# Optimization experiments

Hardware: AMD Instinct MI355X
Metric: run time of the kernel (lower is better)

The kernel has to match this reference:

```python
import jax, jax.numpy as jnp
import numpy as np

N_CELLS, D_IN, D_HID, D_OUT, MLP_W = 16384, 512, 1024, 512, 128
N_FACTIONS, SYNC, DEBATE = 8, 0.15, 0.15


def setup_inputs() -> dict:
    key = jax.random.key(0)
    ks = jax.random.split(key, 20)
    s = 0.05
    inp = {
        "x": jax.random.normal(ks[0], (1, D_IN), jnp.float32),
        "hiddens": jax.random.normal(ks[1], (N_CELLS, D_HID), jnp.float32) * 0.1,
        "wealth_norm": jax.random.uniform(ks[2], (N_CELLS,), jnp.float32, 0.5, 1.5),
        "Wa1": jax.random.normal(ks[3], (D_IN + D_HID, MLP_W), jnp.float32) * s,
        "ba1": jax.random.normal(ks[4], (MLP_W,), jnp.float32) * s,
        "Wa2": jax.random.normal(ks[5], (MLP_W, D_OUT), jnp.float32) * s,
        "ba2": jax.random.normal(ks[6], (D_OUT,), jnp.float32) * s,
        "Wg1": jax.random.normal(ks[7], (D_IN + D_HID, MLP_W), jnp.float32) * s,
        "bg1": jax.random.normal(ks[8], (MLP_W,), jnp.float32) * s,
        "Wg2": jax.random.normal(ks[9], (MLP_W, D_OUT), jnp.float32) * s,
        "bg2": jax.random.normal(ks[10], (D_OUT,), jnp.float32) * s,
        "W_ih": jax.random.normal(ks[11], (D_OUT + 1, 3 * D_HID), jnp.float32) * s,
        "W_hh": jax.random.normal(ks[12], (D_HID, 3 * D_HID), jnp.float32) * s,
        "b_ih": jax.random.normal(ks[13], (3 * D_HID,), jnp.float32) * s,
        "b_hh": jax.random.normal(ks[14], (3 * D_HID,), jnp.float32) * s,
        "Wo": jax.random.normal(ks[15], (D_OUT, D_IN), jnp.float32) * s,
        "bo": jax.random.normal(ks[16], (D_IN,), jnp.float32) * s,
        "positions": jax.random.randint(ks[17], (N_CELLS,), 0, 3, jnp.int32) - 1,
        "step": 10,
    }
    return inp


def _gru_cell(mem, h, W_ih, W_hh, b_ih, b_hh):
    # torch.nn.GRUCell math, gate order r, z, n
    gi = mem @ W_ih + b_ih            # [N, 3H]
    gh = h @ W_hh + b_hh              # [N, 3H]
    gi_r, gi_z, gi_n = jnp.split(gi, 3, axis=-1)
    gh_r, gh_z, gh_n = jnp.split(gh, 3, axis=-1)
    r = jax.nn.sigmoid(gi_r + gh_r)
    z = jax.nn.sigmoid(gi_z + gh_z)
    n = jnp.tanh(gi_n + r * gh_n)
    return (1.0 - z) * n + z * h


def _group_sync(h, mask):
    cnt = jnp.sum(mask)
    m = mask[:, None].astype(h.dtype)
    mean = jnp.sum(h * m, axis=0) / jnp.maximum(cnt, 1).astype(h.dtype)
    blended = 0.9 * h + 0.1 * mean
    return jnp.where((mask[:, None]) & (cnt >= 2), blended, h)


def _faction_sync_debate(h, step):
    n = h.shape[0]
    n_f = min(N_FACTIONS, n // 2)
    if n_f < 2:
        return h
    fs = n // n_f
    hf = h[: n_f * fs].reshape(n_f, fs, -1)
    fmean = hf.mean(axis=1, keepdims=True)                    # [n_f, 1, H]
    hf = (1.0 - SYNC) * hf + SYNC * fmean
    if step > 5:
        global_op = hf.mean(axis=1).mean(axis=0)              # [H]
        dc = max(1, fs // 4)
        head = (1.0 - DEBATE) * hf[:, :dc] + DEBATE * global_op
        hf = jnp.concatenate([head, hf[:, dc:]], axis=1)
    out = hf.reshape(n_f * fs, -1)
    if n_f * fs < n:
        out = jnp.concatenate([out, h[n_f * fs:]], axis=0)
    return out


def reference(x, hiddens, wealth_norm, Wa1, ba1, Wa2, ba2, Wg1, bg1, Wg2, bg2,
              W_ih, W_hh, b_ih, b_hh, Wo, bo, positions, step):
    n = hiddens.shape[0]
    xb = jnp.broadcast_to(x, (n, x.shape[-1]))                # same x for every cell
    combined = jnp.concatenate([xb, hiddens], axis=-1)        # [N, D_in+D_hid]
    a = jax.nn.relu(combined @ Wa1 + ba1) @ Wa2 + ba2
    g = jax.nn.relu(combined @ Wg1 + bg1) @ Wg2 + bg2
    output = a - g                                            # [N, D_out]
    tension = jnp.mean(output ** 2, axis=-1, keepdims=True)   # [N, 1]
    mem_input = jax.lax.stop_gradient(jnp.concatenate([output, tension], axis=-1))
    new_h = _gru_cell(mem_input, hiddens, W_ih, W_hh, b_ih, b_hh)
    mod = 0.9 + 0.1 * jnp.clip(wealth_norm, 0.1, 2.0)
    new_h = jnp.clip(new_h * mod[:, None], -10.0, 10.0)
    new_h = jax.lax.stop_gradient(new_h)                      # original detaches state
    new_h = _group_sync(new_h, positions > 0)
    new_h = _group_sync(new_h, positions < 0)
    new_h = _faction_sync_debate(new_h, step)
    # tension weights come from .item() in torch -> constants
    weights = jax.nn.softmax(jax.lax.stop_gradient(tension[:, 0]))
    combined_out = weights @ output                           # [D_out]
    pred = (combined_out @ Wo + bo)[None, :]                  # [1, D_in]
    avg_tension = jnp.mean(tension)
    return pred, avg_tension, new_h
```

## Files before the change

### kernel.cpp

```cpp
#include <hip/hip_runtime.h>
#include <stdint.h>

typedef unsigned short u16;
typedef __bf16 bf16x8 __attribute__((ext_vector_type(8)));
typedef float f32x4 __attribute__((ext_vector_type(4)));


__device__ __forceinline__ float bf2f(unsigned u) { return __uint_as_float(u << 16); }
__device__ __forceinline__ u16 f2bf(float f) {
  unsigned x = __float_as_uint(f);
  unsigned r = x + 0x7fffu + ((x >> 16) & 1u);
  return (u16)(r >> 16);
}
__device__ __forceinline__ unsigned pack2(float a, float b) {
  return (unsigned)f2bf(a) | ((unsigned)f2bf(b) << 16);
}
__device__ __forceinline__ float sigm(float x) { return 1.f / (1.f + __expf(-x)); }
__device__ __forceinline__ float fast_tanh(float x) {
  float e = __expf(2.f * x);
  return 1.f - 2.f / (e + 1.f);
}

#define AS1(p) ((const __attribute__((address_space(1))) void*)(p))
#define AS3(p) ((__attribute__((address_space(3))) void*)(p))

#define NC 16384

__global__ __launch_bounds__(256) void prep_cvt(const float* __restrict__ hid,
                                                u16* __restrict__ hidc) {
  int b = blockIdx.x, t = threadIdx.x;
  const float4* src = (const float4*)hid;
  uint2* dst = (uint2*)hidc;
#pragma unroll
  for (int c = 0; c < 8; ++c) {
    float4 v = src[(size_t)(b + c * 2048) * 256 + t];
    uint2 o; o.x = pack2(v.x, v.y); o.y = pack2(v.z, v.w);
    dst[(size_t)(b + c * 2048) * 256 + t] = o;
  }
}

__device__ __forceinline__ void packT_body(
    const float* __restrict__ src, int sld, int srow0,
    u16* __restrict__ dst, int dld, int drow0, int koff,
    int remapThresh, int remapAdd, float sgn, int bx, int by,
    float (*tile)[65], int t) {
  const int k0 = by * 64, c0 = bx * 64;
  const int tx = t & 15, ty = t >> 4;
#pragma unroll
  for (int p = 0; p < 4; ++p) {
    int r = ty + p * 16;
    float4 v = *reinterpret_cast<const float4*>(&src[(size_t)(srow0 + k0 + r) * sld + c0 + tx * 4]);
    tile[tx * 4 + 0][r] = v.x;
    tile[tx * 4 + 1][r] = v.y;
    tile[tx * 4 + 2][r] = v.z;
    tile[tx * 4 + 3][r] = v.w;
  }
  __syncthreads();
  const int cl = t >> 2;
  const int kb = (t & 3) * 16;
  int col = c0 + cl;
  int row = drow0 + col + ((col >= remapThresh) ? remapAdd : 0);
  union { u16 o[16]; uint4 v[2]; } u;
#pragma unroll
  for (int e = 0; e < 16; ++e) u.o[e] = f2bf(sgn * tile[cl][kb + e]);
  uint4* d = reinterpret_cast<uint4*>(&dst[(size_t)row * dld + koff + k0 + kb]);
  d[0] = u.v[0]; d[1] = u.v[1];
}

__global__ __launch_bounds__(256) void prep_packT(
    const float* __restrict__ W_ih, const float* __restrict__ W_hh, u16* __restrict__ WgruT,
    const float* __restrict__ Wa1, const float* __restrict__ Wg1, u16* __restrict__ W1catT,
    const float* __restrict__ Wa2, const float* __restrict__ Wg2, u16* __restrict__ W2catT) {
  __shared__ float tile[64][65];
  int b = blockIdx.x, t = threadIdx.x;
  if (b < 768) {
    packT_body(W_hh, 3072, 0, WgruT, 1536, 0, 512, 2048, 1024, 1.f, b % 48, b / 48, tile, t);
    return;
  }
  b -= 768;
  if (b < 384) {
    packT_body(W_ih, 3072, 0, WgruT, 1536, 0, 0, 1 << 30, 0, 1.f, b % 48, b / 48, tile, t);
    return;
  }
  b -= 384;
  if (b < 32) { packT_body(Wa1, 128, 512, W1catT, 1024, 0, 0, 1 << 30, 0, 1.f, b % 2, b / 2, tile, t); return; }
  b -= 32;
  if (b < 32) { packT_body(Wg1, 128, 512, W1catT, 1024, 128, 0, 1 << 30, 0, 1.f, b % 2, b / 2, tile, t); return; }
  b -= 32;
  if (b < 16) { packT_body(Wa2, 512, 0, W2catT, 256, 0, 0, 1 << 30, 0, 1.f, b % 8, b / 8, tile, t); return; }
  b -= 16;
  { packT_body(Wg2, 512, 0, W2catT, 256, 0, 128, 1 << 30, 0, -1.f, b % 8, b / 8, tile, t); }
}

__global__ __launch_bounds__(256) void prep_small(
    const float* __restrict__ Wa1, const float* __restrict__ Wg1,
    const float* __restrict__ x, const float* __restrict__ ba1, const float* __restrict__ bg1,
    float* __restrict__ bias1, const float* __restrict__ ba2, const float* __restrict__ bg2,
    float* __restrict__ bias2, const int* __restrict__ positions, int* __restrict__ counts) {
  int b = blockIdx.x, t = threadIdx.x;
  if (b < 64) {
    const float* W = (t < 128) ? Wa1 : Wg1;
    int cc = t & 127;
    int k0 = b * 8;
    float wv[8], xv[8];
#pragma unroll
    for (int j = 0; j < 8; ++j) {
      xv[j] = x[k0 + j];
      wv[j] = W[(size_t)(k0 + j) * 128 + cc];
    }
    float acc = 0.f;
#pragma unroll
    for (int j = 0; j < 8; ++j) acc += xv[j] * wv[j];
    if (b == 0) acc += (t < 128) ? ba1[cc] : bg1[cc];
    atomicAdd(&bias1[t], acc);
    return;
  }
  b -= 64;
  if (b < 2) { int n = b * 256 + t; bias2[n] = ba2[n] - bg2[n]; return; }
  b -= 2;
  {
    int i = b * 256 + t;
    int p = positions[i], f = i >> 11;
    if (p > 0) atomicAdd(&counts[f * 2], 1);
    else if (p < 0) atomicAdd(&counts[f * 2 + 1], 1);
  }
}

__global__ __launch_bounds__(256) void gemm_bt(
    const u16* __restrict__ A, int lda,
    const u16* __restrict__ Bt, int ldb,
    u16* __restrict__ C, int ldc,
    const float* __restrict__ bias, int epi, int K,
    float* __restrict__ tension) {
  __shared__ __align__(16) u16 As[3][128 * 32];
  __shared__ __align__(16) u16 Bs[3][128 * 32];
  const int tid = threadIdx.x;
  const int m0 = blockIdx.x * 128;
  const int n0 = blockIdx.y * 128;
  f32x4 acc[4][4] = {};
  const int lane = tid & 63;
  const int w = tid >> 6;
  const int mw = (w & 1) * 64, nw = (w >> 1) * 64;
  const int fr = lane & 15;
  const int q = lane >> 4;
  const int ar0 = tid >> 2;
  const int ag = ((tid & 3) ^ ((ar0 >> 1) & 3)) * 8;

  const u16* aB0 = A + (size_t)(m0 + ar0) * lda + ag;
  const u16* aB1 = A + (size_t)(m0 + ar0 + 64) * lda + ag;
  const u16* bB0 = Bt + (size_t)(n0 + ar0) * ldb + ag;
  const u16* bB1 = Bt + (size_t)(n0 + ar0 + 64) * ldb + ag;

  auto stage = [&](int kk, int buf) {
    __builtin_amdgcn_global_load_lds(AS1(aB0 + kk), AS3(&As[buf][tid * 8]), 16, 0, 0);
    __builtin_amdgcn_global_load_lds(AS1(aB1 + kk), AS3(&As[buf][(tid + 256) * 8]), 16, 0, 0);
    __builtin_amdgcn_global_load_lds(AS1(bB0 + kk), AS3(&Bs[buf][tid * 8]), 16, 0, 0);
    __builtin_amdgcn_global_load_lds(AS1(bB1 + kk), AS3(&Bs[buf][(tid + 256) * 8]), 16, 0, 0);
  };

  const int NT = K >> 5;
  stage(0, 0);
  stage(32, 1);
  int cur = 0, nxt = 1, nx2 = 2;
#pragma unroll 1
  for (int t = 0; t < NT; ++t) {
    if (t + 2 < NT) stage((t + 2) * 32, nx2);
    const int rem = NT - 1 - t;
    if (rem >= 2)      asm volatile("s_waitcnt vmcnt(8)" ::: "memory");
    else if (rem == 1) asm volatile("s_waitcnt vmcnt(4)" ::: "memory");
    else               asm volatile("s_waitcnt vmcnt(0)" ::: "memory");
    __builtin_amdgcn_s_barrier();
    asm volatile("" ::: "memory");
    bf16x8 af[4], bfv[4];
#pragma unroll
    for (int mt = 0; mt < 4; ++mt) {
      int r = mw + mt * 16 + fr;
      af[mt] = *reinterpret_cast<const bf16x8*>(&As[cur][r * 32 + ((q ^ ((r >> 1) & 3)) * 8)]);
    }
#pragma unroll
    for (int nt = 0; nt < 4; ++nt) {
      int r = nw + nt * 16 + fr;
      bfv[nt] = *reinterpret_cast<const bf16x8*>(&Bs[cur][r * 32 + ((q ^ ((r >> 1) & 3)) * 8)]);
    }
    __builtin_amdgcn_s_setprio(1);
#pragma unroll
    for (int mt = 0; mt < 4; ++mt)
#pragma unroll
      for (int nt = 0; nt < 4; ++nt)
        acc[mt][nt] = __builtin_amdgcn_mfma_f32_16x16x32_bf16(af[mt], bfv[nt], acc[mt][nt], 0, 0, 0);
    __builtin_amdgcn_s_setprio(0);
    asm volatile("s_waitcnt lgkmcnt(0)" ::: "memory");
    __builtin_amdgcn_s_barrier();
    int tmp = cur; cur = nxt; nxt = nx2; nx2 = tmp;
  }
  const int rq = q * 4;
#pragma unroll
  for (int mt = 0; mt < 4; ++mt) {
    float srow[4] = {0.f, 0.f, 0.f, 0.f};
#pragma unroll
    for (int nt = 0; nt < 4; ++nt) {
      int col = n0 + nw + nt * 16 + fr;
      f32x4 v = acc[mt][nt];
#pragma unroll
      for (int r = 0; r < 4; ++r) {
        int row = m0 + mw + mt * 16 + rq + r;
        float val = v[r] + bias[col];
        if (epi == 1) val = val > 0.f ? val : 0.f;
        else srow[r] += val * val;
        C[(size_t)row * ldc + col] = f2bf(val);
      }
    }
    if (epi == 3) {
#pragma unroll
      for (int r = 0; r < 4; ++r) {
        float s = srow[r];
        s += __shfl_xor(s, 1, 16); s += __shfl_xor(s, 2, 16);
        s += __shfl_xor(s, 4, 16); s += __shfl_xor(s, 8, 16);
        if (fr == 0) atomicAdd(&tension[m0 + mw + mt * 16 + rq + r], s);
      }
    }
  }
}

__global__ __launch_bounds__(256, 2) void gemm_gru(
    const u16* __restrict__ outbf, const u16* __restrict__ hidc,
    const u16* __restrict__ WgruT,
    const float* __restrict__ W_ihf, const float* __restrict__ bihf,
    const float* __restrict__ bhhf, const float* __restrict__ wealthf,
    const float* __restrict__ tension, u16* __restrict__ hpre) {
  __shared__ __align__(16) u16 As[2][128 * 64];
  __shared__ __align__(16) u16 Bs[2][3][64 * 64];
  const int tid = threadIdx.x;
  const int m0 = blockIdx.x * 128;
  const int j0 = blockIdx.y * 64;
  f32x4 acc[4][4][2] = {};
  const int lane = tid & 63;
  const int w = tid >> 6;
  const int mw = (w & 1) * 64, jw = (w >> 1) * 32;
  const int fr = lane & 15;
  const int q = lane >> 4;
  const int rowl = tid >> 3;
  const int koffT = ((tid & 7) ^ (rowl & 7)) * 8;
  const size_t aOutB = (size_t)(m0 + rowl) * 512 + koffT;
  const size_t aHidB = (size_t)(m0 + rowl) * 1024 + koffT;
  const size_t bB    = (size_t)(j0 + rowl) * 1536 + koffT;
  const int f7 = fr & 7;
  const int sk0 = (q ^ f7) * 8;
  const int sk1 = ((4 + q) ^ f7) * 8;

#define STAGE(S, BUF)                                                                              \
  {                                                                                                \
    const int s8 = (S) < 8 ? (S) : (S) - 8;                                                        \
    const size_t kO = (size_t)(S) * 64;                                                            \
    const size_t kOA = (size_t)s8 * 64;                                                            \
    if ((S) < 8) {                                                                                 \
      _Pragma("unroll") for (int it = 0; it < 4; ++it)                                             \
          __builtin_amdgcn_global_load_lds(AS1(outbf + aOutB + (size_t)(32 * it) * 512 + kOA),     \
                                           AS3(&As[BUF][tid * 8 + it * 2048]), 16, 0, 0);          \
    } else {                                                                                       \
      _Pragma("unroll") for (int it = 0; it < 4; ++it)                                             \
          __builtin_amdgcn_global_load_lds(AS1(hidc + aHidB + (size_t)(32 * it) * 1024 + kOA),     \
                                           AS3(&As[BUF][tid * 8 + it * 2048]), 16, 0, 0);          \
    }                                                                                              \
    const u16* bp = WgruT + bB + kO;                                                               \
    __builtin_amdgcn_global_load_lds(AS1(bp), AS3(&Bs[BUF][0][tid * 8]), 16, 0, 0);                \
    __builtin_amdgcn_global_load_lds(AS1(bp + (size_t)32 * 1536),                                  \
                                     AS3(&Bs[BUF][0][tid * 8 + 2048]), 16, 0, 0);                  \
    __builtin_amdgcn_global_load_lds(AS1(bp + (size_t)1024 * 1536),                                \
                                     AS3(&Bs[BUF][1][tid * 8]), 16, 0, 0);                         \
    __builtin_amdgcn_global_load_lds(AS1(bp + (size_t)1056 * 1536),                                \
                                     AS3(&Bs[BUF][1][tid * 8 + 2048]), 16, 0, 0);                  \
    const size_t nOff = ((S) < 8 ? (size_t)2048 * 1536 : (size_t)3072 * 1536);                     \
    __builtin_amdgcn_global_load_lds(AS1(bp + nOff), AS3(&Bs[BUF][2][tid * 8]), 16, 0, 0);         \
    __builtin_amdgcn_global_load_lds(AS1(bp + nOff + (size_t)32 * 1536),                           \
                                     AS3(&Bs[BUF][2][tid * 8 + 2048]), 16, 0, 0);                  \
  }

#define GRU_STEP(T, REG3, CUR)                                                                     \
  {                                                                                                \
    bf16x8 af0[4], b00[2], b10[2], b20[2];                                                         \
    _Pragma("unroll") for (int mt = 0; mt < 4; ++mt)                                               \
        af0[mt] = *reinterpret_cast<const bf16x8*>(&As[CUR][(mw + mt * 16 + fr) * 64 + sk0]);      \
    _Pragma("unroll") for (int nt = 0; nt < 2; ++nt) {                                             \
      int rj = (jw + nt * 16 + fr) * 64 + sk0;                                                     \
      b00[nt] = *reinterpret_cast<const bf16x8*>(&Bs[CUR][0][rj]);                                 \
      b10[nt] = *reinterpret_cast<const bf16x8*>(&Bs[CUR][1][rj]);                                 \
      b20[nt] = *reinterpret_cast<const bf16x8*>(&Bs[CUR][2][rj]);                                 \
    }                                                                                              \
    __builtin_amdgcn_s_setprio(1);                                                                 \
    _Pragma("unroll") for (int mt = 0; mt < 4; ++mt)                                               \
        _Pragma("unroll") for (int nt = 0; nt < 2; ++nt) {                                         \
      acc[0][mt][nt] = __builtin_amdgcn_mfma_f32_16x16x32_bf16(af0[mt], b00[nt], acc[0][mt][nt], 0, 0, 0); \
      acc[1][mt][nt] = __builtin_amdgcn_mfma_f32_16x16x32_bf16(af0[mt], b10[nt], acc[1][mt][nt], 0, 0, 0); \
      acc[REG3][mt][nt] = __builtin_amdgcn_mfma_f32_16x16x32_bf16(af0[mt], b20[nt], acc[REG3][mt][nt], 0, 0, 0); \
    }                                                                                              \
    __builtin_amdgcn_s_setprio(0);                                                                 \
    bf16x8 af1[4], b01[2], b11[2], b21[2];                                                         \
    _Pragma("unroll") for (int mt = 0; mt < 4; ++mt)                                               \
        af1[mt] = *reinterpret_cast<const bf16x8*>(&As[CUR][(mw + mt * 16 + fr) * 64 + sk1]);      \
    _Pragma("unroll") for (int nt = 0; nt < 2; ++nt) {                                             \
      int rj = (jw + nt * 16 + fr) * 64 + sk1;                                                     \
      b01[nt] = *reinterpret_cast<const bf16x8*>(&Bs[CUR][0][rj]);                                 \
      b11[nt] = *reinterpret_cast<const bf16x8*>(&Bs[CUR][1][rj]);                                 \
      b21[nt] = *reinterpret_cast<const bf16x8*>(&Bs[CUR][2][rj]);                                 \
    }                                                                                              \
    asm volatile("s_waitcnt lgkmcnt(0)" ::: "memory");                                             \
    __builtin_amdgcn_s_barrier();                                                                  \
    asm volatile("" ::: "memory");                                                                 \
    if ((T) + 2 < 24) { STAGE((T) + 2, CUR) }                                                      \
    __builtin_amdgcn_s_setprio(1);                                                                 \
    _Pragma("unroll") for (int mt = 0; mt < 4; ++mt)                                               \
        _Pragma("unroll") for (int nt = 0; nt < 2; ++nt) {                                         \
      acc[0][mt][nt] = __builtin_amdgcn_mfma_f32_16x16x32_bf16(af1[mt], b01[nt], acc[0][mt][nt], 0, 0, 0); \
      acc[1][mt][nt] = __builtin_amdgcn_mfma_f32_16x16x32_bf16(af1[mt], b11[nt], acc[1][mt][nt], 0, 0, 0); \
      acc[REG3][mt][nt] = __builtin_amdgcn_mfma_f32_16x16x32_bf16(af1[mt], b21[nt], acc[REG3][mt][nt], 0, 0, 0); \
    }                                                                                              \
    __builtin_amdgcn_s_setprio(0);                                                                 \
    if ((T) + 2 < 24)      { asm volatile("s_waitcnt vmcnt(10)" ::: "memory"); }                   \
    else if ((T) + 1 < 24) { asm volatile("s_waitcnt vmcnt(0)" ::: "memory"); }                    \
    __builtin_amdgcn_s_barrier();                                                                  \
    asm volatile("" ::: "memory");                                                                 \
  }

  STAGE(0, 0)
  STAGE(1, 1)
  asm volatile("s_waitcnt vmcnt(10)" ::: "memory");
  __builtin_amdgcn_s_barrier();
  asm volatile("" ::: "memory");
#pragma unroll 1
  for (int T = 0; T < 8; T += 2) {
    GRU_STEP(T, 2, 0)
    GRU_STEP(T + 1, 2, 1)
  }
#pragma unroll 1
  for (int T = 8; T < 24; T += 2) {
    GRU_STEP(T, 3, 0)
    GRU_STEP(T + 1, 3, 1)
  }
#undef GRU_STEP
#undef STAGE

  const int rq = q * 4;
  const float* wt = W_ihf + (size_t)512 * 3072;
  float wtr[2], wtz[2], wtn[2], bir[2], biz[2], bin_[2], bhr_[2], bhz_[2], bhn_[2];
#pragma unroll
  for (int nt = 0; nt < 2; ++nt) {
    int j = j0 + jw + nt * 16 + fr;
    wtr[nt] = wt[j]; wtz[nt] = wt[1024 + j]; wtn[nt] = wt[2048 + j];
    bir[nt] = bihf[j]; biz[nt] = bihf[1024 + j]; bin_[nt] = bihf[2048 + j];
    bhr_[nt] = bhhf[j]; bhz_[nt] = bhhf[1024 + j]; bhn_[nt] = bhhf[2048 + j];
  }
#pragma unroll
  for (int mt = 0; mt < 4; ++mt) {
#pragma unroll
    for (int rr = 0; rr < 4; ++rr) {
      int row = m0 + mw + mt * 16 + rq + rr;
      float tv = tension[row] * (1.f / 512.f);
      float wl = fminf(fmaxf(wealthf[row], 0.1f), 2.0f);
      float mod = 0.9f + 0.1f * wl;
#pragma unroll
      for (int nt = 0; nt < 2; ++nt) {
        int j = j0 + jw + nt * 16 + fr;
        float r = sigm(acc[0][mt][nt][rr] + tv * wtr[nt] + bir[nt] + bhr_[nt]);
        float z = sigm(acc[1][mt][nt][rr] + tv * wtz[nt] + biz[nt] + bhz_[nt]);
        float n = fast_tanh(acc[2][mt][nt][rr] + tv * wtn[nt] + bin_[nt]
                            + r * (acc[3][mt][nt][rr] + bhn_[nt]));
        float h = bf2f(hidc[(size_t)row * 1024 + j]);
        float h2 = (1.f - z) * n + z * h;
        h2 = fminf(fmaxf(h2 * mod, -10.f), 10.f);
        hpre[(size_t)row * 1024 + j] = f2bf(h2);
      }
    }
  }
}

__global__ void stats_kernel(const u16* __restrict__ hpre, const int* __restrict__ positions,
                             float* __restrict__ fsums) {
  int cc = blockIdx.x, f = blockIdx.y, z = blockIdx.z, t = threadIdx.x;
  int col = cc * 128 + (t & 127);
  int half = t >> 7;
  float st = 0, sp = 0, sm = 0;
  for (int it = 0; it < 128; ++it) {
    int row = (f << 11) + ((z * 128 + it) << 1) + half;
    int p = positions[row];
    float v = bf2f(hpre[(size_t)row * 1024 + col]);
    st += v;
    if (p > 0) sp += v;
    if (p < 0) sm += v;
  }
  atomicAdd(&fsums[(f * 3 + 0) * 1024 + col], st);
  atomicAdd(&fsums[(f * 3 + 1) * 1024 + col], sp);
  atomicAdd(&fsums[(f * 3 + 2) * 1024 + col], sm);
}

__global__ void derive_kernel(const float* __restrict__ fsums, const int* __restrict__ counts,
                              float* __restrict__ mean1, float* __restrict__ mean2,
                              float* __restrict__ fmean, float* __restrict__ gop,
                              float* __restrict__ scal) {
  int c = threadIdx.x;
  int cnt1 = 0, cnt2 = 0, cf1[8], cf2[8];
#pragma unroll
  for (int f = 0; f < 8; ++f) {
    cf1[f] = counts[f * 2]; cf2[f] = counts[f * 2 + 1];
    cnt1 += cf1[f]; cnt2 += cf2[f];
  }
  float s1 = 0, s2 = 0;
#pragma unroll
  for (int f = 0; f < 8; ++f) { s1 += fsums[(f * 3 + 1) * 1024 + c]; s2 += fsums[(f * 3 + 2) * 1024 + c]; }
  float m1 = s1 / (float)(cnt1 > 1 ? cnt1 : 1);
  float m2 = s2 / (float)(cnt2 > 1 ? cnt2 : 1);
  float a1 = (cnt1 >= 2) ? 0.1f : 0.f;
  float a2 = (cnt2 >= 2) ? 0.1f : 0.f;
  float g = 0;
#pragma unroll
  for (int f = 0; f < 8; ++f) {
    float fm = (fsums[(f * 3) * 1024 + c]
                + a1 * ((float)cf1[f] * m1 - fsums[(f * 3 + 1) * 1024 + c])
                + a2 * ((float)cf2[f] * m2 - fsums[(f * 3 + 2) * 1024 + c])) * (1.f / 2048.f);
    fmean[f * 1024 + c] = fm;
    g += fm;
  }
  gop[c] = g * 0.125f;
  mean1[c] = m1; mean2[c] = m2;
  if (c == 0) { scal[0] = a1; scal[1] = a2; }
}

__global__ void finalize_kernel(const u16* __restrict__ hpre, const int* __restrict__ positions,
                                const int* __restrict__ step, const float* __restrict__ mean1,
                                const float* __restrict__ mean2, const float* __restrict__ fmean,
                                const float* __restrict__ gop, const float* __restrict__ scal,
                                float* __restrict__ out) {
  int t = threadIdx.x;
  int r0 = blockIdx.x * 8;
  float s0 = scal[0], s1 = scal[1];
  bool step5 = step[0] > 5;
#pragma unroll 2
  for (int rr = 0; rr < 8; ++rr) {
    int row = r0 + rr;
    int p = positions[row];
    float w1 = (p > 0) ? s0 : 0.f;
    float w2 = (p < 0) ? s1 : 0.f;
    int f = row >> 11, qq = row & 2047;
    bool deb = step5 && (qq < 512);
    const u16* hrow = hpre + (size_t)row * 1024;
    const float* fmp = fmean + f * 1024;
    float* orow = out + 513 + (size_t)row * 1024;
#pragma unroll
    for (int e = 0; e < 4; ++e) {
      int c = e * 256 + t;
      float h = bf2f(hrow[c]);
      float hgs = h + w1 * (mean1[c] - h) + w2 * (mean2[c] - h);
      float hfs = 0.85f * hgs + 0.15f * fmp[c];
      orow[c] = deb ? (0.85f * hfs + 0.15f * gop[c]) : hfs;
    }
  }
}

__global__ void softmax_kernel(const float* __restrict__ tension, float* __restrict__ weights,
                               float* __restrict__ out) {
  __shared__ float red[1024];
  int t = threadIdx.x;
  float tv[16], mx = -1e30f, sumt = 0.f;
#pragma unroll
  for (int k = 0; k < 16; ++k) {
    tv[k] = tension[t + k * 1024] * (1.f / 512.f);
    mx = fmaxf(mx, tv[k]); sumt += tv[k];
  }
  red[t] = mx; __syncthreads();
  for (int s = 512; s > 0; s >>= 1) { if (t < s) red[t] = fmaxf(red[t], red[t + s]); __syncthreads(); }
  float m = red[0]; __syncthreads();
  red[t] = sumt; __syncthreads();
  for (int s = 512; s > 0; s >>= 1) { if (t < s) red[t] += red[t + s]; __syncthreads(); }
  float tot = red[0]; __syncthreads();
  float ev[16], se = 0.f;
#pragma unroll
  for (int k = 0; k < 16; ++k) { ev[k] = __expf(tv[k] - m); se += ev[k]; }
  red[t] = se; __syncthreads();
  for (int s = 512; s > 0; s >>= 1) { if (t < s) red[t] += red[t + s]; __syncthreads(); }
  float invS = 1.f / red[0];
#pragma unroll
  for (int k = 0; k < 16; ++k) weights[t + k * 1024] = ev[k] * invS;
  if (t == 0) out[512] = tot * (1.f / 16384.f);
}

__global__ void wsum_kernel(const float* __restrict__ weights, const u16* __restrict__ outbf,
                            float* __restrict__ co) {
  int b = blockIdx.x, t = threadIdx.x;
  int c = t * 2;
  float a0 = 0.f, a1 = 0.f;
  int i0 = b * 128;
  for (int i = i0; i < i0 + 128; ++i) {
    float w = weights[i];
    unsigned v = *reinterpret_cast<const unsigned*>(outbf + (size_t)i * 512 + c);
    a0 += w * bf2f(v & 0xffff);
    a1 += w * bf2f(v >> 16);
  }
  atomicAdd(&co[c], a0);
  atomicAdd(&co[c + 1], a1);
}

__global__ void pred_kernel(const float* __restrict__ co, const float* __restrict__ Wof,
                            const float* __restrict__ bof, float* __restrict__ out) {
  __shared__ float cs[512];
  int t = threadIdx.x, n = blockIdx.x * 256 + t;
  cs[t] = co[t]; cs[t + 256] = co[t + 256];
  __syncthreads();
  float acc = bof[n];
  for (int ck = 0; ck < 512; ++ck) acc += cs[ck] * Wof[(size_t)ck * 512 + n];
  out[n] = acc;
}

extern "C" void kernel_launch(void* const* d_in, const int* in_sizes, int n_in,
                              void* d_out, int out_size, void* d_ws, size_t ws_size,
                              hipStream_t stream) {
  const float* x      = (const float*)d_in[0];
  const float* hid    = (const float*)d_in[1];
  const float* wealth = (const float*)d_in[2];
  const float* Wa1    = (const float*)d_in[3];
  const float* ba1    = (const float*)d_in[4];
  const float* Wa2    = (const float*)d_in[5];
  const float* ba2    = (const float*)d_in[6];
  const float* Wg1    = (const float*)d_in[7];
  const float* bg1    = (const float*)d_in[8];
  const float* Wg2    = (const float*)d_in[9];
  const float* bg2    = (const float*)d_in[10];
  const float* W_ih   = (const float*)d_in[11];
  const float* W_hh   = (const float*)d_in[12];
  const float* b_ih   = (const float*)d_in[13];
  const float* b_hh   = (const float*)d_in[14];
  const float* Wo     = (const float*)d_in[15];
  const float* bo     = (const float*)d_in[16];
  const int* positions= (const int*)d_in[17];
  const int* step     = (const int*)d_in[18];
  float* out = (float*)d_out;

  char* w = (char*)d_ws;
  size_t off = 0;
  auto alloc = [&](size_t bytes) { void* p = w + off; off += (bytes + 255) & ~(size_t)255; return p; };
  u16*   hidc    = (u16*)  alloc((size_t)NC * 1024 * 2);
  u16*   outbf   = (u16*)  alloc((size_t)NC * 512 * 2);
  u16*   hpre    = (u16*)  alloc((size_t)NC * 1024 * 2);
  u16*   WgruT   = (u16*)  alloc((size_t)4096 * 1536 * 2);
  u16*   W1catT  = (u16*)  alloc((size_t)256 * 1024 * 2);
  u16*   W2catT  = (u16*)  alloc((size_t)512 * 256 * 2);
  u16*   t1      = (u16*)  alloc((size_t)NC * 256 * 2);
  float* bias1   = (float*)alloc(256 * 4);
  float* co      = (float*)alloc(512 * 4);
  int*   counts  = (int*)  alloc(16 * 4);
  float* fsums   = (float*)alloc(8 * 3 * 1024 * 4);
  float* tension = (float*)alloc(NC * 4);
  float* bias2   = (float*)alloc(512 * 4);
  float* weights = (float*)alloc(NC * 4);
  float* mean1   = (float*)alloc(1024 * 4);
  float* mean2   = (float*)alloc(1024 * 4);
  float* gop     = (float*)alloc(1024 * 4);
  float* fmean   = (float*)alloc(8 * 1024 * 4);
  float* scal    = (float*)alloc(8 * 4);

  (void)hipMemsetAsync(bias1, 0, 1024 + 2048 + 256 + 98304 + 65536, stream);

  prep_small<<<130, 256, 0, stream>>>(Wa1, Wg1, x, ba1, bg1, bias1, ba2, bg2, bias2,
                                      positions, counts);
  prep_cvt<<<2048, 256, 0, stream>>>(hid, hidc);
  prep_packT<<<1248, 256, 0, stream>>>(W_ih, W_hh, WgruT, Wa1, Wg1, W1catT,
                                       Wa2, Wg2, W2catT);

  gemm_bt<<<dim3(128, 2), 256, 0, stream>>>(hidc, 1024, W1catT, 1024, t1, 256,
                                            bias1, 1, 1024, nullptr);
  gemm_bt<<<dim3(128, 4), 256, 0, stream>>>(t1, 256, W2catT, 256, outbf, 512,
                                            bias2, 3, 256, tension);

  gemm_gru<<<dim3(128, 16), 256, 0, stream>>>(outbf, hidc, WgruT, W_ih, b_ih, b_hh,
                                              wealth, tension, hpre);

  stats_kernel<<<dim3(8, 8, 8), 256, 0, stream>>>(hpre, positions, fsums);
  derive_kernel<<<1, 1024, 0, stream>>>(fsums, counts, mean1, mean2, fmean, gop, scal);
  finalize_kernel<<<2048, 256, 0, stream>>>(hpre, positions, step, mean1, mean2, fmean, gop,
                                            scal, out);

  softmax_kernel<<<1, 1024, 0, stream>>>(tension, weights, out);
  wsum_kernel<<<128, 256, 0, stream>>>(weights, outbf, co);
  pred_kernel<<<2, 256, 0, stream>>>(co, Wo, bo, out);

  (void)in_sizes; (void)n_in; (void)out_size; (void)ws_size;
}
```

Before: 570.6 us.

## Halve GRU GEMM K-step to shrink LDS and raise occupancy

The fused GRU GEMM now stages K in chunks of 32 instead of 64, using a packed LDS layout: each 64-element LDS row holds two tile rows' 32-wide K slices, and each wave selects its half through a swizzled column offset. This halves the shared-memory footprint so launch bounds can request 4 blocks per CU instead of 2, trading more pipeline steps and barriers (48 instead of 24) for more latency hiding. The higher occupancy target squeezes the register budget while the kernel keeps 128 accumulator floats per thread, so spills are a risk.

```diff
diff --git a/kernel.cpp b/kernel.cpp
--- a/kernel.cpp
+++ b/kernel.cpp
@@ -222,14 +222,14 @@
   }
 }
 
-__global__ __launch_bounds__(256, 2) void gemm_gru(
+__global__ __launch_bounds__(256, 4) void gemm_gru(
     const u16* __restrict__ outbf, const u16* __restrict__ hidc,
     const u16* __restrict__ WgruT,
     const float* __restrict__ W_ihf, const float* __restrict__ bihf,
     const float* __restrict__ bhhf, const float* __restrict__ wealthf,
     const float* __restrict__ tension, u16* __restrict__ hpre) {
-  __shared__ __align__(16) u16 As[2][128 * 64];
-  __shared__ __align__(16) u16 Bs[2][3][64 * 64];
+  __shared__ __align__(16) u16 As[2][64 * 64];
+  __shared__ __align__(16) u16 Bs[2][3][32 * 64];
   const int tid = threadIdx.x;
   const int m0 = blockIdx.x * 128;
   const int j0 = blockIdx.y * 64;
@@ -239,101 +239,83 @@
   const int mw = (w & 1) * 64, jw = (w >> 1) * 32;
   const int fr = lane & 15;
   const int q = lane >> 4;
-  const int rowl = tid >> 3;
-  const int koffT = ((tid & 7) ^ (rowl & 7)) * 8;
-  const size_t aOutB = (size_t)(m0 + rowl) * 512 + koffT;
-  const size_t aHidB = (size_t)(m0 + rowl) * 1024 + koffT;
-  const size_t bB    = (size_t)(j0 + rowl) * 1536 + koffT;
   const int f7 = fr & 7;
-  const int sk0 = (q ^ f7) * 8;
-  const int sk1 = ((4 + q) ^ f7) * 8;
+  const int skA = ((q + (w & 1) * 4) ^ f7) * 8;
+  const int skB = ((q + (w >> 1) * 4) ^ f7) * 8;
+  const int rl = tid >> 3;
+  const int sidx = (tid & 7) ^ (rl & 7);
+  const int kcol = (sidx & 3) * 8;
+  const int ah = (sidx >= 4) ? 64 : 0;
+  const int bh = (sidx >= 4) ? 32 : 0;
+  const size_t aOut1 = (size_t)(m0 + rl + ah) * 512 + kcol;
+  const size_t aOut2 = aOut1 + (size_t)32 * 512;
+  const size_t aHid1 = (size_t)(m0 + rl + ah) * 1024 + kcol;
+  const size_t aHid2 = aHid1 + (size_t)32 * 1024;
+  const size_t bBase = (size_t)(j0 + rl + bh) * 1536 + kcol;
 
 #define STAGE(S, BUF)                                                                              \
   {                                                                                                \
-    const int s8 = (S) < 8 ? (S) : (S) - 8;                                                        \
-    const size_t kO = (size_t)(S) * 64;                                                            \
-    const size_t kOA = (size_t)s8 * 64;                                                            \
-    if ((S) < 8) {                                                                                 \
-      _Pragma("unroll") for (int it = 0; it < 4; ++it)                                             \
-          __builtin_amdgcn_global_load_lds(AS1(outbf + aOutB + (size_t)(32 * it) * 512 + kOA),     \
-                                           AS3(&As[BUF][tid * 8 + it * 2048]), 16, 0, 0);          \
+    const int sA = (S) < 16 ? (S) : (S) - 16;                                                      \
+    const size_t kOA = (size_t)sA * 32;                                                            \
+    const size_t kOB = (size_t)(S) * 32;                                                           \
+    if ((S) < 16) {                                                                                \
+      __builtin_amdgcn_global_load_lds(AS1(outbf + aOut1 + kOA), AS3(&As[BUF][tid * 8]), 16, 0, 0);\
+      __builtin_amdgcn_global_load_lds(AS1(outbf + aOut2 + kOA),                                   \
+                                       AS3(&As[BUF][2048 + tid * 8]), 16, 0, 0);                   \
     } else {                                                                                       \
-      _Pragma("unroll") for (int it = 0; it < 4; ++it)                                             \
-          __builtin_amdgcn_global_load_lds(AS1(hidc + aHidB + (size_t)(32 * it) * 1024 + kOA),     \
-                                           AS3(&As[BUF][tid * 8 + it * 2048]), 16, 0, 0);          \
+      __builtin_amdgcn_global_load_lds(AS1(hidc + aHid1 + kOA), AS3(&As[BUF][tid * 8]), 16, 0, 0); \
+      __builtin_amdgcn_global_load_lds(AS1(hidc + aHid2 + kOA),                                    \
+                                       AS3(&As[BUF][2048 + tid * 8]), 16, 0, 0);                   \
     }                                                                                              \
-    const u16* bp = WgruT + bB + kO;                                                               \
+    const u16* bp = WgruT + bBase + kOB;                                                           \
     __builtin_amdgcn_global_load_lds(AS1(bp), AS3(&Bs[BUF][0][tid * 8]), 16, 0, 0);                \
-    __builtin_amdgcn_global_load_lds(AS1(bp + (size_t)32 * 1536),                                  \
-                                     AS3(&Bs[BUF][0][tid * 8 + 2048]), 16, 0, 0);                  \
     __builtin_amdgcn_global_load_lds(AS1(bp + (size_t)1024 * 1536),                                \
                                      AS3(&Bs[BUF][1][tid * 8]), 16, 0, 0);                         \
-    __builtin_amdgcn_global_load_lds(AS1(bp + (size_t)1056 * 1536),                                \
-                                     AS3(&Bs[BUF][1][tid * 8 + 2048]), 16, 0, 0);                  \
-    const size_t nOff = ((S) < 8 ? (size_t)2048 * 1536 : (size_t)3072 * 1536);                     \
-    __builtin_amdgcn_global_load_lds(AS1(bp + nOff), AS3(&Bs[BUF][2][tid * 8]), 16, 0, 0);         \
-    __builtin_amdgcn_global_load_lds(AS1(bp + nOff + (size_t)32 * 1536),                           \
-                                     AS3(&Bs[BUF][2][tid * 8 + 2048]), 16, 0, 0);                  \
+    __builtin_amdgcn_global_load_lds(AS1(bp + (size_t)((S) < 16 ? 2048 : 3072) * 1536),            \
+                                     AS3(&Bs[BUF][2][tid * 8]), 16, 0, 0);                         \
   }
 
 #define GRU_STEP(T, REG3, CUR)                                                                     \
   {                                                                                                \
-    bf16x8 af0[4], b00[2], b10[2], b20[2];                                                         \
+    bf16x8 af[4], b0v[2], b1v[2], b2v[2];                                                          \
     _Pragma("unroll") for (int mt = 0; mt < 4; ++mt)                                               \
-        af0[mt] = *reinterpret_cast<const bf16x8*>(&As[CUR][(mw + mt * 16 + fr) * 64 + sk0]);      \
+        af[mt] = *reinterpret_cast<const bf16x8*>(&As[CUR][(mt * 16 + fr) * 64 + skA]);            \
     _Pragma("unroll") for (int nt = 0; nt < 2; ++nt) {                                             \
-      int rj = (jw + nt * 16 + fr) * 64 + sk0;                                                     \
-      b00[nt] = *reinterpret_cast<const bf16x8*>(&Bs[CUR][0][rj]);                                 \
-      b10[nt] = *reinterpret_cast<const bf16x8*>(&Bs[CUR][1][rj]);                                 \
-      b20[nt] = *reinterpret_cast<const bf16x8*>(&Bs[CUR][2][rj]);                                 \
-    }                                                                                              \
-    __builtin_amdgcn_s_setprio(1);                                                                 \
-    _Pragma("unroll") for (int mt = 0; mt < 4; ++mt)                                               \
-        _Pragma("unroll") for (int nt = 0; nt < 2; ++nt) {                                         \
-      acc[0][mt][nt] = __builtin_amdgcn_mfma_f32_16x16x32_bf16(af0[mt], b00[nt], acc[0][mt][nt], 0, 0, 0); \
-      acc[1][mt][nt] = __builtin_amdgcn_mfma_f32_16x16x32_bf16(af0[mt], b10[nt], acc[1][mt][nt], 0, 0, 0); \
-      acc[REG3][mt][nt] = __builtin_amdgcn_mfma_f32_16x16x32_bf16(af0[mt], b20[nt], acc[REG3][mt][nt], 0, 0, 0); \
-    }                                                                                              \
-    __builtin_amdgcn_s_setprio(0);                                                                 \
-    bf16x8 af1[4], b01[2], b11[2], b21[2];                                                         \
-    _Pragma("unroll") for (int mt = 0; mt < 4; ++mt)                                               \
-        af1[mt] = *reinterpret_cast<const bf16x8*>(&As[CUR][(mw + mt * 16 + fr) * 64 + sk1]);      \
-    _Pragma("unroll") for (int nt = 0; nt < 2; ++nt) {                                             \
-      int rj = (jw + nt * 16 + fr) * 64 + sk1;                                                     \
-      b01[nt] = *reinterpret_cast<const bf16x8*>(&Bs[CUR][0][rj]);                                 \
-      b11[nt] = *reinterpret_cast<const bf16x8*>(&Bs[CUR][1][rj]);                                 \
-      b21[nt] = *reinterpret_cast<const bf16x8*>(&Bs[CUR][2][rj]);                                 \
+      int rj = (nt * 16 + fr) * 64 + skB;                                                          \
+      b0v[nt] = *reinterpret_cast<const bf16x8*>(&Bs[CUR][0][rj]);                                 \
+      b1v[nt] = *reinterpret_cast<const bf16x8*>(&Bs[CUR][1][rj]);                                 \
+      b2v[nt] = *reinterpret_cast<const bf16x8*>(&Bs[CUR][2][rj]);                                 \
     }                                                                                              \
     asm volatile("s_waitcnt lgkmcnt(0)" ::: "memory");                                             \
     __builtin_amdgcn_s_barrier();                                                                  \
     asm volatile("" ::: "memory");                                                                 \
-    if ((T) + 2 < 24) { STAGE((T) + 2, CUR) }                                                      \
+    if ((T) + 2 < 48) { STAGE((T) + 2, CUR) }                                                      \
     __builtin_amdgcn_s_setprio(1);                                                                 \
     _Pragma("unroll") for (int mt = 0; mt < 4; ++mt)                                               \
         _Pragma("unroll") for (int nt = 0; nt < 2; ++nt) {                                         \
-      acc[0][mt][nt] = __builtin_amdgcn_mfma_f32_16x16x32_bf16(af1[mt], b01[nt], acc[0][mt][nt], 0, 0, 0); \
-      acc[1][mt][nt] = __builtin_amdgcn_mfma_f32_16x16x32_bf16(af1[mt], b11[nt], acc[1][mt][nt], 0, 0, 0); \
-      acc[REG3][mt][nt] = __builtin_amdgcn_mfma_f32_16x16x32_bf16(af1[mt], b21[nt], acc[REG3][mt][nt], 0, 0, 0); \
+      acc[0][mt][nt] = __builtin_amdgcn_mfma_f32_16x16x32_bf16(af[mt], b0v[nt], acc[0][mt][nt], 0, 0, 0); \
+      acc[1][mt][nt] = __builtin_amdgcn_mfma_f32_16x16x32_bf16(af[mt], b1v[nt], acc[1][mt][nt], 0, 0, 0); \
+      acc[REG3][mt][nt] = __builtin_amdgcn_mfma_f32_16x16x32_bf16(af[mt], b2v[nt], acc[REG3][mt][nt], 0, 0, 0); \
     }                                                                                              \
     __builtin_amdgcn_s_setprio(0);                                                                 \
-    if ((T) + 2 < 24)      { asm volatile("s_waitcnt vmcnt(10)" ::: "memory"); }                   \
-    else if ((T) + 1 < 24) { asm volatile("s_waitcnt vmcnt(0)" ::: "memory"); }                    \
+    if ((T) + 2 < 48)      { asm volatile("s_waitcnt vmcnt(5)" ::: "memory"); }                    \
+    else if ((T) + 1 < 48) { asm volatile("s_waitcnt vmcnt(0)" ::: "memory"); }                    \
     __builtin_amdgcn_s_barrier();                                                                  \
     asm volatile("" ::: "memory");                                                                 \
   }
 
   STAGE(0, 0)
   STAGE(1, 1)
-  asm volatile("s_waitcnt vmcnt(10)" ::: "memory");
+  asm volatile("s_waitcnt vmcnt(5)" ::: "memory");
   __builtin_amdgcn_s_barrier();
   asm volatile("" ::: "memory");
 #pragma unroll 1
-  for (int T = 0; T < 8; T += 2) {
+  for (int T = 0; T < 16; T += 2) {
     GRU_STEP(T, 2, 0)
     GRU_STEP(T + 1, 2, 1)
   }
 #pragma unroll 1
-  for (int T = 8; T < 24; T += 2) {
+  for (int T = 16; T < 48; T += 2) {
     GRU_STEP(T, 3, 0)
     GRU_STEP(T + 1, 3, 1)
   }
```

Result: slower. 1.432 ms (+151.0%).
